# Kernel tuning notes

Hardware: AMD Instinct MI355X
Metric: run time of the kernel (lower is better)

Reference implementation:

```python
import jax, jax.numpy as jnp
import numpy as np

B, T, V, E, H, O = 64, 2048, 50000, 256, 256, 16

def setup_inputs() -> dict:
    key = jax.random.key(0)
    ks = jax.random.split(key, 10)
    s_rnn = 1.0 / np.sqrt(H)
    s_fc1 = 1.0 / np.sqrt(H)
    s_fc2 = 1.0 / np.sqrt(H // 2)
    return {
        "x": jax.random.randint(ks[0], (B, T), 0, V, dtype=jnp.int32),
        "emb": jax.random.normal(ks[1], (V, E), dtype=jnp.float32),
        "W_ih": jax.random.uniform(ks[2], (H, E), jnp.float32, -s_rnn, s_rnn),
        "W_hh": jax.random.uniform(ks[3], (H, H), jnp.float32, -s_rnn, s_rnn),
        "b_ih": jax.random.uniform(ks[4], (H,), jnp.float32, -s_rnn, s_rnn),
        "b_hh": jax.random.uniform(ks[5], (H,), jnp.float32, -s_rnn, s_rnn),
        "fc1_w": jax.random.uniform(ks[6], (H // 2, H), jnp.float32, -s_fc1, s_fc1),
        "fc1_b": jax.random.uniform(ks[7], (H // 2,), jnp.float32, -s_fc1, s_fc1),
        "fc2_w": jax.random.uniform(ks[8], (O, H // 2), jnp.float32, -s_fc2, s_fc2),
        "fc2_b": jax.random.uniform(ks[9], (O,), jnp.float32, -s_fc2, s_fc2),
    }

def reference(x, emb, W_ih, W_hh, b_ih, b_hh, fc1_w, fc1_b, fc2_w, fc2_b):
    # Embedding lookup: [B, T, E]
    e = emb[x]
    # Precompute input-to-hidden projection for all timesteps in one big GEMM
    xh = jnp.einsum("bte,he->bth", e, W_ih) + b_ih + b_hh  # [B, T, H]
    h0 = jnp.zeros((x.shape[0], W_hh.shape[0]), dtype=e.dtype)

    def step(h, xt):  # h: [B, H], xt: [B, H]
        h = jnp.tanh(xt + h @ W_hh.T)
        return h, None

    h_last, _ = jax.lax.scan(step, h0, jnp.swapaxes(xh, 0, 1))  # final hidden [B, H]
    # Dropout is identity at inference. MLP head: fc1 -> relu -> fc2
    hid = jax.nn.relu(h_last @ fc1_w.T + fc1_b)
    return hid @ fc2_w.T + fc2_b  # [B, O]
```

## Files before the change

kernel.cpp:

```cpp
#include <hip/hip_runtime.h>
#include <hip/hip_bf16.h>


#define B_  64
#define T_  2048
#define E_  256
#define H_  256
#define O_  16
#define H2_ 128
#define CH  2
#define HP  264

typedef _Float16 f16x2 __attribute__((ext_vector_type(2)));
typedef _Float16 f16x4 __attribute__((ext_vector_type(4)));
typedef _Float16 f16x8 __attribute__((ext_vector_type(8)));
typedef float    f32x2 __attribute__((ext_vector_type(2)));
typedef float    f32x4 __attribute__((ext_vector_type(4)));

#define LDS_BARRIER() asm volatile("s_waitcnt lgkmcnt(0)\n\ts_barrier" ::: "memory")

__device__ __forceinline__ float tanh_fast(float x) {
  const float e = __expf(2.0f * x);
  return fmaf(-2.0f, __builtin_amdgcn_rcpf(e + 1.0f), 1.0f);
}

__global__ __launch_bounds__(256) void k0_cvt(
    const float* __restrict__ W_ih, const float* __restrict__ W_hh,
    _Float16* __restrict__ Wih16, _Float16* __restrict__ Whh16) {
  const int i = (blockIdx.x * 256 + threadIdx.x) * 4;
  if (i < H_ * E_) {
    float4 a = *(const float4*)&W_ih[i];
    float4 b = *(const float4*)&W_hh[i];
    f16x4 ah, bh;
    ah[0]=(_Float16)a.x; ah[1]=(_Float16)a.y; ah[2]=(_Float16)a.z; ah[3]=(_Float16)a.w;
    bh[0]=(_Float16)b.x; bh[1]=(_Float16)b.y; bh[2]=(_Float16)b.z; bh[3]=(_Float16)b.w;
    *(f16x4*)&Wih16[i] = ah;
    *(f16x4*)&Whh16[i] = bh;
  }
}

__global__ __launch_bounds__(256) void k1_xh(
    const int* __restrict__ x, const float* __restrict__ emb,
    const _Float16* __restrict__ Wih16, const float* __restrict__ b_ih,
    const float* __restrict__ b_hh, _Float16* __restrict__ xh) {
  __shared__ _Float16 A16[64][264];
  const int tid  = threadIdx.x;
  const int w    = tid >> 6;
  const int lane = tid & 63;
  const int nl   = lane & 15;
  const int koff = (lane >> 4) << 3;
  const long r0  = (long)blockIdx.x * 64;

  {
    const int c4 = lane << 2;
#pragma unroll
    for (int it = 0; it < 16; ++it) {
      const int row = (it << 2) + w;
      const long tok = x[r0 + row];
      const float4 v = *(const float4*)&emb[tok * E_ + c4];
      f16x4 hv;
      hv[0] = (_Float16)v.x; hv[1] = (_Float16)v.y;
      hv[2] = (_Float16)v.z; hv[3] = (_Float16)v.w;
      *(f16x4*)&A16[row][c4] = hv;
    }
  }

  f16x8 bfr[4][8];
#pragma unroll
  for (int nt = 0; nt < 4; ++nt) {
    const int n = (w << 6) + (nt << 4) + nl;
#pragma unroll
    for (int kt = 0; kt < 8; ++kt)
      bfr[nt][kt] = *(const f16x8*)&Wih16[n * E_ + (kt << 5) + koff];
  }
  __syncthreads();

  f32x4 acc[4][4];
#pragma unroll
  for (int mt = 0; mt < 4; ++mt)
#pragma unroll
    for (int nt = 0; nt < 4; ++nt) acc[mt][nt] = (f32x4){};

#pragma unroll
  for (int mt = 0; mt < 4; ++mt) {
#pragma unroll
    for (int kt = 0; kt < 8; ++kt) {
      const f16x8 a = *(const f16x8*)&A16[(mt << 4) + nl][(kt << 5) + koff];
#pragma unroll
      for (int nt = 0; nt < 4; ++nt)
        acc[mt][nt] = __builtin_amdgcn_mfma_f32_16x16x32_f16(a, bfr[nt][kt], acc[mt][nt], 0, 0, 0);
    }
  }
  __syncthreads();

  {
    const int rsub = (lane >> 4) << 2;
#pragma unroll
    for (int nt = 0; nt < 4; ++nt) {
      const int n = (w << 6) + (nt << 4) + nl;
      const float bias = b_ih[n] + b_hh[n];
#pragma unroll
      for (int mt = 0; mt < 4; ++mt)
#pragma unroll
        for (int j = 0; j < 4; ++j)
          A16[(mt << 4) + rsub + j][n] = (_Float16)(acc[mt][nt][j] + bias);
    }
  }
  __syncthreads();

  {
#pragma unroll
    for (int i = 0; i < 8; ++i) {
      const int row = (w << 4) + (i << 1) + (lane >> 5);
      const int col = (lane & 31) << 3;
      *(f16x8*)&xh[(r0 + row) * H_ + col] = *(const f16x8*)&A16[row][col];
    }
  }
}

__global__ __launch_bounds__(256, 1) void k2_rnn(
    const _Float16* __restrict__ xh, const _Float16* __restrict__ Whh16,
    const float* __restrict__ fc1_w, const float* __restrict__ fc1_b,
    const float* __restrict__ fc2_w, const float* __restrict__ fc2_b,
    float* __restrict__ out) {
  __shared__ _Float16 h16[2][CH][HP];
  __shared__ float    sc[CH][264];
  __shared__ float    hid_s[CH][H2_ + 4];

  const int tid  = threadIdx.x;
  const int w    = tid >> 6;
  const int lane = tid & 63;
  const int nl   = lane & 15;
  const int quad = lane >> 4;
  const int cc   = nl & 1;
  const int koff = quad << 3;
  const int c0   = blockIdx.x * CH;
  const int pc   = tid >> 7;
  const int po   = (tid & 127) << 1;

  f16x8 afr[4][8];
#pragma unroll
  for (int mt = 0; mt < 4; ++mt) {
    const int i = (w << 6) + (mt << 4) + nl;
#pragma unroll
    for (int kt = 0; kt < 8; ++kt)
      afr[mt][kt] = *(const f16x8*)&Whh16[i * H_ + (kt << 5) + koff];
  }

  if (tid < 66) *(f16x8*)&(((_Float16*)h16[0])[tid << 3]) = (f16x8){};

  const _Float16* xb = xh + (size_t)(c0 + pc) * T_ * H_ + po;
  f16x2 xq[4], xn[4];
#pragma unroll
  for (int s = 0; s < 4; ++s) xq[s] = *(const f16x2*)&xb[(size_t)s * H_];
#pragma unroll
  for (int s = 0; s < 4; ++s) xn[s] = *(const f16x2*)&xb[(size_t)(4 + s) * H_];
  __syncthreads();

#define STEP(RB, WB, S)                                                        \
  {                                                                            \
    f16x8 bfr[8];                                                              \
    _Pragma("unroll")                                                          \
    for (int kt = 0; kt < 8; ++kt)                                             \
      bfr[kt] = *(const f16x8*)&h16[RB][cc][(kt << 5) + koff];                 \
    const f32x4 zz = {};                                                       \
    _Pragma("unroll")                                                          \
    for (int mt = 0; mt < 4; ++mt) {                                           \
      f32x4 a0 = __builtin_amdgcn_mfma_f32_16x16x32_f16(afr[mt][0], bfr[0], zz, 0, 0, 0); \
      a0       = __builtin_amdgcn_mfma_f32_16x16x32_f16(afr[mt][1], bfr[1], a0, 0, 0, 0); \
      a0       = __builtin_amdgcn_mfma_f32_16x16x32_f16(afr[mt][2], bfr[2], a0, 0, 0, 0); \
      a0       = __builtin_amdgcn_mfma_f32_16x16x32_f16(afr[mt][3], bfr[3], a0, 0, 0, 0); \
      f32x4 a1 = __builtin_amdgcn_mfma_f32_16x16x32_f16(afr[mt][4], bfr[4], zz, 0, 0, 0); \
      a1       = __builtin_amdgcn_mfma_f32_16x16x32_f16(afr[mt][5], bfr[5], a1, 0, 0, 0); \
      a1       = __builtin_amdgcn_mfma_f32_16x16x32_f16(afr[mt][6], bfr[6], a1, 0, 0, 0); \
      a1       = __builtin_amdgcn_mfma_f32_16x16x32_f16(afr[mt][7], bfr[7], a1, 0, 0, 0); \
      const f32x4 sm = a0 + a1;                                                \
      if (nl < CH)                                                             \
        *(f32x4*)&sc[nl][(w << 6) + (mt << 4) + (quad << 2)] = sm;             \
    }                                                                          \
    LDS_BARRIER();                                                             \
    {                                                                          \
      const f32x2 sv = *(const f32x2*)&sc[pc][po];                             \
      f16x2 o;                                                                 \
      o[0] = (_Float16)tanh_fast(sv[0] + (float)xq[S][0]);                     \
      o[1] = (_Float16)tanh_fast(sv[1] + (float)xq[S][1]);                     \
      *(f16x2*)&h16[WB][pc][po] = o;                                           \
    }                                                                          \
    LDS_BARRIER();                                                             \
  }

  for (int tt = 0; tt < T_; tt += 4) {
    STEP(0, 1, 0)
    STEP(1, 0, 1)
    STEP(0, 1, 2)
    STEP(1, 0, 3)
#pragma unroll
    for (int s = 0; s < 4; ++s) xq[s] = xn[s];
    const int tn = tt + 8;
#pragma unroll
    for (int s = 0; s < 4; ++s) {
      const size_t ti = (size_t)((tn + s) & (T_ - 1)) * H_;
      xn[s] = *(const f16x2*)&xb[ti];
    }
  }
#undef STEP

  __syncthreads();

  {
    const int o = tid & 127;
    float s = fc1_b[o];
#pragma unroll 8
    for (int k = 0; k < H_; ++k) s += fc1_w[o * H_ + k] * (float)h16[0][pc][k];
    hid_s[pc][o] = fmaxf(s, 0.f);
  }
  __syncthreads();
  if (tid < CH * O_) {
    const int c = tid >> 4, o = tid & 15;
    float s = fc2_b[o];
#pragma unroll 8
    for (int k = 0; k < H2_; ++k) s += fc2_w[o * H2_ + k] * hid_s[c][k];
    out[(size_t)(c0 + c) * O_ + o] = s;
  }
}

extern "C" void kernel_launch(void* const* d_in, const int* in_sizes, int n_in,
                              void* d_out, int out_size, void* d_ws, size_t ws_size,
                              hipStream_t stream) {
  const int*   x     = (const int*)d_in[0];
  const float* emb   = (const float*)d_in[1];
  const float* W_ih  = (const float*)d_in[2];
  const float* W_hh  = (const float*)d_in[3];
  const float* b_ih  = (const float*)d_in[4];
  const float* b_hh  = (const float*)d_in[5];
  const float* fc1_w = (const float*)d_in[6];
  const float* fc1_b = (const float*)d_in[7];
  const float* fc2_w = (const float*)d_in[8];
  const float* fc2_b = (const float*)d_in[9];
  float* outp = (float*)d_out;

  _Float16* xh16  = (_Float16*)d_ws;
  _Float16* Wih16 = xh16 + (size_t)B_ * T_ * H_;
  _Float16* Whh16 = Wih16 + (size_t)H_ * E_;

  k0_cvt<<<dim3(H_ * E_ / 1024), dim3(256), 0, stream>>>(W_ih, W_hh, Wih16, Whh16);
  k1_xh<<<dim3(B_ * T_ / 64), dim3(256), 0, stream>>>(x, emb, Wih16, b_ih, b_hh, xh16);
  k2_rnn<<<dim3(B_ / CH), dim3(256), 0, stream>>>(xh16, Whh16, fc1_w, fc1_b, fc2_w, fc2_b, outp);
}
```

Baseline: 1.569 ms.

## Apply tanh in MFMA registers and drop the scratch LDS round-trip and barrier

Each lane now selects its own tile of the MFMA accumulator and applies the bias add and tanh directly in registers. Lanes with nl < 8 write the new hidden values straight into the h16 double buffer. This removes the sc scratch buffer, one LDS write/read pair and one barrier per recurrent step, which shortens the serial critical path. In exchange, each lane computes tanh for 4 values, redundantly across lanes, and fetches x in f16x4 chunks with a different access pattern.

```diff
diff --git a/kernel.cpp b/kernel.cpp
--- a/kernel.cpp
+++ b/kernel.cpp
@@ -11,10 +11,8 @@
 #define CH  2
 #define HP  264
 
-typedef _Float16 f16x2 __attribute__((ext_vector_type(2)));
 typedef _Float16 f16x4 __attribute__((ext_vector_type(4)));
 typedef _Float16 f16x8 __attribute__((ext_vector_type(8)));
-typedef float    f32x2 __attribute__((ext_vector_type(2)));
 typedef float    f32x4 __attribute__((ext_vector_type(4)));
 
 #define LDS_BARRIER() asm volatile("s_waitcnt lgkmcnt(0)\n\ts_barrier" ::: "memory")
@@ -124,7 +122,6 @@
     const float* __restrict__ fc2_w, const float* __restrict__ fc2_b,
     float* __restrict__ out) {
   __shared__ _Float16 h16[2][CH][HP];
-  __shared__ float    sc[CH][264];
   __shared__ float    hid_s[CH][H2_ + 4];
 
   const int tid  = threadIdx.x;
@@ -133,10 +130,10 @@
   const int nl   = lane & 15;
   const int quad = lane >> 4;
   const int cc   = nl & 1;
+  const int mts  = (nl >> 1) & 3;
   const int koff = quad << 3;
+  const int rowb = (w << 6) + (mts << 4) + (quad << 2);
   const int c0   = blockIdx.x * CH;
-  const int pc   = tid >> 7;
-  const int po   = (tid & 127) << 1;
 
   f16x8 afr[4][8];
 #pragma unroll
@@ -149,12 +146,12 @@
 
   if (tid < 66) *(f16x8*)&(((_Float16*)h16[0])[tid << 3]) = (f16x8){};
 
-  const _Float16* xb = xh + (size_t)(c0 + pc) * T_ * H_ + po;
-  f16x2 xq[4], xn[4];
-#pragma unroll
-  for (int s = 0; s < 4; ++s) xq[s] = *(const f16x2*)&xb[(size_t)s * H_];
-#pragma unroll
-  for (int s = 0; s < 4; ++s) xn[s] = *(const f16x2*)&xb[(size_t)(4 + s) * H_];
+  const _Float16* xb = xh + (size_t)(c0 + cc) * T_ * H_ + rowb;
+  f16x4 xq[4], xn[4];
+#pragma unroll
+  for (int s = 0; s < 4; ++s) xq[s] = *(const f16x4*)&xb[(size_t)s * H_];
+#pragma unroll
+  for (int s = 0; s < 4; ++s) xn[s] = *(const f16x4*)&xb[(size_t)(4 + s) * H_];
   __syncthreads();
 
 #define STEP(RB, WB, S)                                                        \
@@ -164,6 +161,7 @@
     for (int kt = 0; kt < 8; ++kt)                                             \
       bfr[kt] = *(const f16x8*)&h16[RB][cc][(kt << 5) + koff];                 \
     const f32x4 zz = {};                                                       \
+    f32x4 sm[4];                                                               \
     _Pragma("unroll")                                                          \
     for (int mt = 0; mt < 4; ++mt) {                                           \
       f32x4 a0 = __builtin_amdgcn_mfma_f32_16x16x32_f16(afr[mt][0], bfr[0], zz, 0, 0, 0); \
@@ -174,18 +172,16 @@
       a1       = __builtin_amdgcn_mfma_f32_16x16x32_f16(afr[mt][5], bfr[5], a1, 0, 0, 0); \
       a1       = __builtin_amdgcn_mfma_f32_16x16x32_f16(afr[mt][6], bfr[6], a1, 0, 0, 0); \
       a1       = __builtin_amdgcn_mfma_f32_16x16x32_f16(afr[mt][7], bfr[7], a1, 0, 0, 0); \
-      const f32x4 sm = a0 + a1;                                                \
-      if (nl < CH)                                                             \
-        *(f32x4*)&sc[nl][(w << 6) + (mt << 4) + (quad << 2)] = sm;             \
+      sm[mt] = a0 + a1;                                                        \
     }                                                                          \
-    LDS_BARRIER();                                                             \
-    {                                                                          \
-      const f32x2 sv = *(const f32x2*)&sc[pc][po];                             \
-      f16x2 o;                                                                 \
-      o[0] = (_Float16)tanh_fast(sv[0] + (float)xq[S][0]);                     \
-      o[1] = (_Float16)tanh_fast(sv[1] + (float)xq[S][1]);                     \
-      *(f16x2*)&h16[WB][pc][po] = o;                                           \
-    }                                                                          \
+    f32x4 ss = sm[0];                                                          \
+    _Pragma("unroll")                                                          \
+    for (int m = 1; m < 4; ++m) if (mts == m) ss = sm[m];                      \
+    f16x4 o;                                                                   \
+    _Pragma("unroll")                                                          \
+    for (int j = 0; j < 4; ++j)                                                \
+      o[j] = (_Float16)tanh_fast(ss[j] + (float)xq[S][j]);                     \
+    if (nl < 8) *(f16x4*)&h16[WB][cc][rowb] = o;                               \
     LDS_BARRIER();                                                             \
   }
 
@@ -200,7 +196,7 @@
 #pragma unroll
     for (int s = 0; s < 4; ++s) {
       const size_t ti = (size_t)((tn + s) & (T_ - 1)) * H_;
-      xn[s] = *(const f16x2*)&xb[ti];
+      xn[s] = *(const f16x4*)&xb[ti];
     }
   }
 #undef STEP
@@ -208,7 +204,8 @@
   __syncthreads();
 
   {
-    const int o = tid & 127;
+    const int pc = tid >> 7;
+    const int o  = tid & 127;
     float s = fc1_b[o];
 #pragma unroll 8
     for (int k = 0; k < H_; ++k) s += fc1_w[o * H_ + k] * (float)h16[0][pc][k];
```

New measurement: 1.376 ms. 12.3% less time.
